# Kernel optimization log

Hardware: AMD Instinct MI355X
Metric: run time of the kernel (lower is better)

## Reference

```python
import jax, jax.numpy as jnp
import numpy as np

K = 9          # neighbors kept after dilation
DILATION = 2   # top-k runs with K*DILATION then strided slice
EPS = 1e-12    # F.normalize eps


def setup_inputs() -> dict:
    key = jax.random.key(0)
    # x: [B, C, N, 1] feature map over N points with C channels
    x = jax.random.normal(key, (2, 64, 8192, 1), dtype=jnp.float32)
    return {"x": x}


def reference(x):
    k_total = K * DILATION
    # L2-normalize along channel dim (F.normalize(x, p=2, dim=1))
    norm = jnp.sqrt(jnp.sum(x * x, axis=1, keepdims=True))
    xn = x / jnp.maximum(norm, EPS)
    # [B, C, N, 1] -> [B, N, C]
    pts = jnp.transpose(jnp.squeeze(xn, -1), (0, 2, 1))
    B, N, _ = pts.shape
    # pairwise squared distances: ||xi||^2 - 2 xi.xj + ||xj||^2  -> [B, N, N]
    sq = jnp.sum(pts * pts, axis=-1, keepdims=True)            # [B, N, 1]
    dist = sq - 2.0 * jnp.einsum('bnc,bmc->bnm', pts, pts) + jnp.swapaxes(sq, 1, 2)
    # k nearest = top-k of negated distance (matches torch.topk(-dist, k))
    _, nn_idx = jax.lax.top_k(-dist, k_total)                  # [B, N, k_total] int32
    center_idx = jnp.broadcast_to(jnp.arange(N, dtype=nn_idx.dtype)[None, :, None],
                                  (B, N, k_total))
    edge_index = jnp.stack([nn_idx, center_idx], axis=0)       # [2, B, N, k_total]
    # dilation (non-stochastic path): strided slice over neighbor dim
    return edge_index[:, :, :, ::DILATION]                     # [2, B, N, K]
```

## Files before the change

kernel.cpp:

```cpp
#include <hip/hip_runtime.h>


#define NPTS  8192
#define CHN   64
#define NB    2
#define KF    18
#define KC    8
#define KM    16
#define KOUT  9
#define NPART 4
#define TPB   32

typedef unsigned u32;
typedef unsigned short u16;
typedef unsigned long long u64;
typedef __attribute__((ext_vector_type(4))) unsigned u32x4;
typedef __attribute__((ext_vector_type(8))) short bf16x8;
typedef __attribute__((ext_vector_type(4))) float f32x4;

__device__ __forceinline__ u32 umin32(u32 a, u32 b) { return a < b ? a : b; }

__device__ __forceinline__ u32 mono32(float f) {
  const u32 u = __float_as_uint(f);
  const u32 s = (u32)((int)u >> 31);
  return u ^ (s | 0x80000000u);
}

__device__ __forceinline__ u32 med3u(u32 a, u32 b, u32 c) {
  u32 r;
  asm("v_med3_u32 %0, %1, %2, %3" : "=v"(r) : "v"(a), "v"(b), "v"(c));
  return r;
}

template <int KK>
__device__ __forceinline__ void insmm(u32 key, u32 (&d)[KK]) {
#pragma unroll
  for (int k = KK - 1; k >= 1; --k) d[k] = med3u(d[k - 1], d[k], key);
  d[0] = umin32(d[0], key);
}

template <int KK>
__device__ __forceinline__ void ins64(u64 key, u64 (&d)[KK]) {
  if (key < d[KK - 1]) {
#pragma unroll
    for (int k = KK - 1; k >= 1; --k) {
      const bool up = d[k - 1] > key;
      const bool here = (!up) && (d[k] > key);
      d[k] = up ? d[k - 1] : (here ? key : d[k]);
    }
    if (d[0] > key) d[0] = key;
  }
}

__device__ __forceinline__ void gload_lds16(const u32* g, u32* l) {
  __builtin_amdgcn_global_load_lds(
      (const __attribute__((address_space(1))) u32*)g,
      (__attribute__((address_space(3))) u32*)l, 16, 0, 0);
}

__device__ __forceinline__ void np_normalize(const float* __restrict__ xb,
                                             float (&v)[CHN]) {
  float ss = 0.f;
#pragma unroll
  for (int c = 0; c < CHN; ++c) {
    v[c] = xb[(size_t)c * NPTS];
    ss = __fadd_rn(ss, __fmul_rn(v[c], v[c]));
  }
  const float den = fmaxf(__fsqrt_rn(ss), 1e-12f);
#pragma unroll
  for (int c = 0; c < CHN; ++c) v[c] = __fdiv_rn(v[c], den);
}

__global__ __launch_bounds__(128) void prep_kernel(
    const float* __restrict__ x, u32* __restrict__ hib, u32* __restrict__ lob,
    u32* __restrict__ w16b, float* __restrict__ sq) {
  const int b = blockIdx.x >> 6;
  const int n = ((blockIdx.x & 63) << 7) + threadIdx.x;
  const int g = (b << 13) + n;
  float v[CHN];
  np_normalize(x + (size_t)b * CHN * NPTS + n, v);
  float r[8];
#pragma unroll
  for (int j = 0; j < 8; ++j) r[j] = __fmul_rn(v[j], v[j]);
#pragma unroll
  for (int blk = 1; blk < 8; ++blk)
#pragma unroll
    for (int j = 0; j < 8; ++j)
      r[j] = __fadd_rn(r[j], __fmul_rn(v[8 * blk + j], v[8 * blk + j]));
  const float t0 = __fadd_rn(r[0], r[1]);
  const float t1 = __fadd_rn(r[2], r[3]);
  const float t2 = __fadd_rn(r[4], r[5]);
  const float t3 = __fadd_rn(r[6], r[7]);
  sq[g] = __fadd_rn(__fadd_rn(t0, t1), __fadd_rn(t2, t3));
  u32* hd = hib + (size_t)g * 32;
  u32* ld = lob + (size_t)g * 32;
  u32* wd = w16b + (size_t)g * 32;
  const int key = n & 7;
#pragma unroll
  for (int q = 0; q < 8; ++q) {
    u32 h[4], l[4], w[4];
#pragma unroll
    for (int p2 = 0; p2 < 4; ++p2) {
      const float a = v[8 * q + 2 * p2];
      const float c = v[8 * q + 2 * p2 + 1];
      const u32 ba = __float_as_uint(a), bc = __float_as_uint(c);
      const float la = a - __uint_as_float(ba & 0xffff0000u);
      const float lc = c - __uint_as_float(bc & 0xffff0000u);
      h[p2] = __builtin_amdgcn_perm(bc, ba, 0x07060302u);
      l[p2] = __builtin_amdgcn_perm(__float_as_uint(lc), __float_as_uint(la),
                                    0x07060302u);
      w[p2] = __builtin_amdgcn_perm(bc, ba, 0x05040100u);
    }
    const int pq = (q ^ key) << 2;
    *(u32x4*)(hd + pq) = (u32x4){h[0], h[1], h[2], h[3]};
    *(u32x4*)(ld + pq) = (u32x4){l[0], l[1], l[2], l[3]};
    *(u32x4*)(wd + pq) = (u32x4){w[0], w[1], w[2], w[3]};
  }
}

__global__ __launch_bounds__(256, 2) void knn_part_kernel(
    const u32* __restrict__ hib, const u32* __restrict__ lob,
    const float* __restrict__ sq, u16* __restrict__ cand) {
  __shared__ __align__(16) u32 pw[4][2][2048];

  const int tid = threadIdx.x;
  const int vb = ((blockIdx.x & 7) << 7) + (blockIdx.x >> 3);
  const int part = vb >> 8;
  const int w = vb & 255;
  const int b = w >> 7;
  const int qbase = (w & 127) << 6;
  const int t_lo = part << 5;
  const u32* __restrict__ hb_ = hib + ((size_t)b << 18);
  const u32* __restrict__ lb_ = lob + ((size_t)b << 18);
  const float* __restrict__ sqb = sq + (b << 13);

  const int lane = tid & 63, wid = tid >> 6;
  const int qoff = (wid & 1) << 5;
  const int moff = (wid >> 1) << 5;
  const int l15 = lane & 15;
  const int h4 = lane >> 4;
  const int sw = l15 & 7;
  const int lofs = lane << 2;

#define STAGE(BUF, TILE)                                                     \
  {                                                                          \
    const u32* sH_ = hb_ + ((size_t)(TILE) << 11) + (moff << 5);             \
    const u32* sL_ = lb_ + ((size_t)(TILE) << 11) + (moff << 5);             \
    u32* bp_ = &pw[wid][(BUF)][0];                                           \
    gload_lds16(sH_ + lofs, bp_ + lofs);                                     \
    gload_lds16(sH_ + 256 + lofs, bp_ + 256 + lofs);                         \
    gload_lds16(sH_ + 512 + lofs, bp_ + 512 + lofs);                         \
    gload_lds16(sH_ + 768 + lofs, bp_ + 768 + lofs);                         \
    gload_lds16(sL_ + lofs, bp_ + 1024 + lofs);                              \
    gload_lds16(sL_ + 256 + lofs, bp_ + 1280 + lofs);                        \
    gload_lds16(sL_ + 512 + lofs, bp_ + 1536 + lofs);                        \
    gload_lds16(sL_ + 768 + lofs, bp_ + 1792 + lofs);                        \
  }

  STAGE(0, t_lo)
  float sqn0 = sqb[(t_lo << 6) + moff + l15];
  float sqn1 = sqb[(t_lo << 6) + moff + 16 + l15];

  bf16x8 ah[2][2], al[2][2];
#pragma unroll
  for (int g = 0; g < 2; ++g)
#pragma unroll
    for (int s = 0; s < 2; ++s) {
      const int row = qbase + qoff + (g << 4) + l15;
      const int off = row * 32 + ((((s << 2) + h4) ^ sw) << 2);
      u32x4 hv = *(const u32x4*)(hb_ + off);
      u32x4 lv = *(const u32x4*)(lb_ + off);
      hv.x ^= 0x80008000u; hv.y ^= 0x80008000u;
      hv.z ^= 0x80008000u; hv.w ^= 0x80008000u;
      lv.x ^= 0x80008000u; lv.y ^= 0x80008000u;
      lv.z ^= 0x80008000u; lv.w ^= 0x80008000u;
      ah[g][s] = __builtin_bit_cast(bf16x8, hv);
      al[g][s] = __builtin_bit_cast(bf16x8, lv);
    }
  asm volatile("s_waitcnt vmcnt(0)" ::: "memory");
  __builtin_amdgcn_sched_barrier(0);

  u32 d[2][4][KC];
#pragma unroll
  for (int g = 0; g < 2; ++g)
#pragma unroll
    for (int i = 0; i < 4; ++i)
#pragma unroll
      for (int k = 0; k < KC; ++k) d[g][i][k] = 0xffffffffu;

  for (int tau = 0; tau < TPB; ++tau) {
    const int cur = tau & 1;
    const float sq0 = sqn0, sq1 = sqn1;
    if (tau + 1 < TPB) {
      STAGE(cur ^ 1, t_lo + tau + 1)
      sqn0 = sqb[((t_lo + tau + 1) << 6) + moff + l15];
      sqn1 = sqb[((t_lo + tau + 1) << 6) + moff + 16 + l15];
      asm volatile("s_waitcnt vmcnt(10)" ::: "memory");
    } else {
      asm volatile("s_waitcnt vmcnt(0)" ::: "memory");
    }
    __builtin_amdgcn_sched_barrier(0);

    const u32* ppc = &pw[wid][cur][0];
#pragma unroll
    for (int f = 0; f < 2; ++f) {
      const float sqm = ((f ? sq1 : sq0) + 2.f) * 0.5f;
      const int rloc = (f << 4) + l15;
      f32x4 acc[2];
      acc[0] = (f32x4){sqm, sqm, sqm, sqm};
      acc[1] = acc[0];
#pragma unroll
      for (int s = 0; s < 2; ++s) {
        const u32* hp = ppc + rloc * 32 + ((((s << 2) + h4) ^ sw) << 2);
        const bf16x8 bh = __builtin_bit_cast(bf16x8, *(const u32x4*)hp);
        const bf16x8 bl = __builtin_bit_cast(bf16x8, *(const u32x4*)(hp + 1024));
        acc[0] = __builtin_amdgcn_mfma_f32_16x16x32_bf16(ah[0][s], bh, acc[0], 0, 0, 0);
        acc[1] = __builtin_amdgcn_mfma_f32_16x16x32_bf16(ah[1][s], bh, acc[1], 0, 0, 0);
        acc[0] = __builtin_amdgcn_mfma_f32_16x16x32_bf16(al[0][s], bh, acc[0], 0, 0, 0);
        acc[1] = __builtin_amdgcn_mfma_f32_16x16x32_bf16(al[1][s], bh, acc[1], 0, 0, 0);
        acc[0] = __builtin_amdgcn_mfma_f32_16x16x32_bf16(ah[0][s], bl, acc[0], 0, 0, 0);
        acc[1] = __builtin_amdgcn_mfma_f32_16x16x32_bf16(ah[1][s], bl, acc[1], 0, 0, 0);
      }
      const u32 lidx = (u32)((tau << 6) + moff + rloc);
#pragma unroll
      for (int g = 0; g < 2; ++g)
#pragma unroll
        for (int i = 0; i < 4; ++i) {
          const u32 keyv = (__float_as_uint(acc[g][i]) & 0xfffff000u) | lidx;
          insmm<KC>(keyv, d[g][i]);
        }
    }
  }
#undef STAGE
  __syncthreads();

  u32* mg = &pw[0][0][0];
  const int stream = ((wid >> 1) << 4) + l15;
  const int rcb = ((wid & 1) << 4) + (h4 << 2);
#pragma unroll
  for (int chunk = 0; chunk < 2; ++chunk) {
#pragma unroll
    for (int i = 0; i < 4; ++i) {
      u32* wr = mg + ((rcb + i) * 32 + stream) * 8;
      u32x4 a, c;
      a.x = d[chunk][i][0]; a.y = d[chunk][i][1];
      a.z = d[chunk][i][2]; a.w = d[chunk][i][3];
      c.x = d[chunk][i][4]; c.y = d[chunk][i][5];
      c.z = d[chunk][i][6]; c.w = d[chunk][i][7];
      *(u32x4*)wr = a;
      *(u32x4*)(wr + 4) = c;
    }
    __syncthreads();
    {
      const int rowc = tid >> 3, oct = tid & 7;
      u32* base = mg + rowc * 256 + oct * 32;
      u32 m1[14];
#pragma unroll
      for (int k = 0; k < 14; ++k) m1[k] = 0xffffffffu;
#pragma unroll
      for (int j = 0; j < 8; ++j) {
        const u32x4 k4 = *(const u32x4*)(base + (j << 2));
        insmm<14>(k4.x, m1);
        insmm<14>(k4.y, m1);
        insmm<14>(k4.z, m1);
        insmm<14>(k4.w, m1);
      }
#pragma unroll
      for (int k = 0; k < 14; ++k) base[k] = m1[k];
    }
    __syncthreads();
    if (tid < 64) {
      const int rowc = tid >> 1, half = tid & 1;
      u32* rb = mg + rowc * 256 + half * 128;
      u32 m2[KM];
#pragma unroll
      for (int k = 0; k < KM; ++k) m2[k] = 0xffffffffu;
#pragma unroll
      for (int o = 0; o < 4; ++o) {
        const u32* p = rb + o * 32;
        for (int j = 0; j < 14; ++j) insmm<KM>(p[j], m2);
      }
#pragma unroll
      for (int k = 0; k < KM; ++k) rb[k] = m2[k];
    }
    __syncthreads();
    if (tid < 32) {
      u32 m3[KM];
#pragma unroll
      for (int k = 0; k < KM; ++k) m3[k] = 0xffffffffu;
      const u32* p0 = mg + tid * 256;
      for (int j = 0; j < KM; ++j) insmm<KM>(p0[j], m3);
      const u32* p1 = mg + tid * 256 + 128;
      for (int j = 0; j < KM; ++j) insmm<KM>(p1[j], m3);
      const int row = ((tid >> 4) << 5) + (chunk << 4) + (tid & 15);
      const int rg = (b << 13) + qbase + row;
      u16* cw = cand + (size_t)rg * (NPART * KM) + part * KM;
#pragma unroll
      for (int k = 0; k < KM; ++k)
        cw[k] = (u16)((part << 11) + (m3[k] & 0xfffu));
    }
    __syncthreads();
  }
}

__global__ __launch_bounds__(512) void finalize_kernel(
    const u32* __restrict__ hib, const u32* __restrict__ w16b,
    const float* __restrict__ sq, const u16* __restrict__ cand,
    int* __restrict__ out) {
  __shared__ u64 ex[64 * 66];
  __shared__ u64 hf[128 * 19];
  const int tid = threadIdx.x;
  const int rl = tid >> 3, sub = tid & 7;
  const int row = (blockIdx.x << 6) + rl;
  const int b = row >> 13;
  const int n = row & 8191;
  const float sqn = sq[row];
  const float* __restrict__ sqb = sq + (b << 13);
  const u32* __restrict__ hb_ = hib + ((size_t)b << 18);
  const u32* __restrict__ wb_ = w16b + ((size_t)b << 18);
  float vq[CHN];
  {
    const u32* hq = hb_ + ((size_t)n << 5);
    const u32* wq = wb_ + ((size_t)n << 5);
    const int key = n & 7;
#pragma unroll
    for (int q = 0; q < 8; ++q) {
      const int pq = (q ^ key) << 2;
      const u32x4 hw = *(const u32x4*)(hq + pq);
      const u32x4 ww = *(const u32x4*)(wq + pq);
      const u32 hv[4] = {hw.x, hw.y, hw.z, hw.w};
      const u32 wv[4] = {ww.x, ww.y, ww.z, ww.w};
#pragma unroll
      for (int p2 = 0; p2 < 4; ++p2) {
        vq[8 * q + 2 * p2] =
            __uint_as_float((hv[p2] << 16) | (wv[p2] & 0xffffu));
        vq[8 * q + 2 * p2 + 1] =
            __uint_as_float((hv[p2] & 0xffff0000u) | (wv[p2] >> 16));
      }
    }
  }
  const u16* __restrict__ cr = cand + (size_t)row * 64 + sub * 8;
  u64* exw = ex + rl * 66 + sub * 8;
  for (int j = 0; j < 8; ++j) {
    const int ix = cr[j];
    const u32* hp = hb_ + ((size_t)ix << 5);
    const u32* wp = wb_ + ((size_t)ix << 5);
    const int key = ix & 7;
    float dot = 0.f;
#pragma unroll
    for (int q = 0; q < 8; ++q) {
      const int pq = (q ^ key) << 2;
      const u32x4 hw = *(const u32x4*)(hp + pq);
      const u32x4 ww = *(const u32x4*)(wp + pq);
      const u32 hv[4] = {hw.x, hw.y, hw.z, hw.w};
      const u32 wv[4] = {ww.x, ww.y, ww.z, ww.w};
#pragma unroll
      for (int p2 = 0; p2 < 4; ++p2) {
        const float a = __uint_as_float((hv[p2] << 16) | (wv[p2] & 0xffffu));
        const float c = __uint_as_float((hv[p2] & 0xffff0000u) | (wv[p2] >> 16));
        dot = __fadd_rn(dot, __fmul_rn(vq[8 * q + 2 * p2], a));
        dot = __fadd_rn(dot, __fmul_rn(vq[8 * q + 2 * p2 + 1], c));
      }
    }
    const float dist =
        __fadd_rn(__fsub_rn(sqn, __fmul_rn(2.0f, dot)), sqb[ix]);
    exw[j] = ((u64)mono32(dist) << 32) | (u32)ix;
  }
  __syncthreads();
  if (tid < 128) {
    const int r2 = tid >> 1, hv = tid & 1;
    u64 m18[KF];
#pragma unroll
    for (int k = 0; k < KF; ++k) m18[k] = ~0ull;
    const u64* p = ex + r2 * 66 + hv * 32;
    for (int j = 0; j < 32; ++j) ins64<KF>(p[j], m18);
    u64* wr = hf + tid * 19;
#pragma unroll
    for (int k = 0; k < KF; ++k) wr[k] = m18[k];
  }
  __syncthreads();
  if (tid < 64) {
    u64 m18[KF];
#pragma unroll
    for (int k = 0; k < KF; ++k) m18[k] = ~0ull;
    const u64* p0 = hf + (tid << 1) * 19;
    const u64* p1 = hf + ((tid << 1) + 1) * 19;
    for (int j = 0; j < KF; ++j) ins64<KF>(p0[j], m18);
    for (int j = 0; j < KF; ++j) ins64<KF>(p1[j], m18);
    const int row2 = (blockIdx.x << 6) + tid;
    int* o0 = out + (size_t)row2 * KOUT;
    int* o1 = o0 + NB * NPTS * KOUT;
#pragma unroll
    for (int k = 0; k < KOUT; ++k) {
      o0[k] = (int)(m18[2 * k] & 0xffffffffu);
      o1[k] = row2 & 8191;
    }
  }
}

extern "C" void kernel_launch(void* const* d_in, const int* in_sizes, int n_in,
                              void* d_out, int out_size, void* d_ws, size_t ws_size,
                              hipStream_t stream) {
  const float* x = (const float*)d_in[0];
  u32* hib = (u32*)d_ws;
  u32* lob = hib + (size_t)NB * NPTS * 32;
  u32* w16b = lob + (size_t)NB * NPTS * 32;
  float* sqg = (float*)(w16b + (size_t)NB * NPTS * 32);
  u16* cand = (u16*)(sqg + NB * NPTS);
  int* out = (int*)d_out;
  prep_kernel<<<dim3(128), dim3(128), 0, stream>>>(x, hib, lob, w16b, sqg);
  knn_part_kernel<<<dim3(1024), dim3(256), 0, stream>>>(hib, lob, sqg, cand);
  finalize_kernel<<<dim3(256), dim3(512), 0, stream>>>(hib, w16b, sqg, cand, out);
}
```

Before: 210.1 us.

## Load candidate tiles directly from global memory into registers, dropping LDS staging

Removes the double-buffered global_load_lds staging of candidate point tiles and the XOR swizzle layout. MFMA B operands and squared norms are now loaded straight from global memory (L2-cached) into registers each iteration. The shared buffer shrinks to the merge area only, and launch bounds allow three blocks per CU to raise occupancy. The cost is that global load latency is no longer hidden by explicit prefetch, and every wave re-reads the tiles through the cache.

```diff
diff --git a/kernel.cpp b/kernel.cpp
--- a/kernel.cpp
+++ b/kernel.cpp
@@ -50,12 +50,6 @@
     }
     if (d[0] > key) d[0] = key;
   }
-}
-
-__device__ __forceinline__ void gload_lds16(const u32* g, u32* l) {
-  __builtin_amdgcn_global_load_lds(
-      (const __attribute__((address_space(1))) u32*)g,
-      (__attribute__((address_space(3))) u32*)l, 16, 0, 0);
 }
 
 __device__ __forceinline__ void np_normalize(const float* __restrict__ xb,
@@ -95,7 +89,6 @@
   u32* hd = hib + (size_t)g * 32;
   u32* ld = lob + (size_t)g * 32;
   u32* wd = w16b + (size_t)g * 32;
-  const int key = n & 7;
 #pragma unroll
   for (int q = 0; q < 8; ++q) {
     u32 h[4], l[4], w[4];
@@ -111,17 +104,17 @@
                                     0x07060302u);
       w[p2] = __builtin_amdgcn_perm(bc, ba, 0x05040100u);
     }
-    const int pq = (q ^ key) << 2;
+    const int pq = q << 2;
     *(u32x4*)(hd + pq) = (u32x4){h[0], h[1], h[2], h[3]};
     *(u32x4*)(ld + pq) = (u32x4){l[0], l[1], l[2], l[3]};
     *(u32x4*)(wd + pq) = (u32x4){w[0], w[1], w[2], w[3]};
   }
 }
 
-__global__ __launch_bounds__(256, 2) void knn_part_kernel(
+__global__ __launch_bounds__(256, 3) void knn_part_kernel(
     const u32* __restrict__ hib, const u32* __restrict__ lob,
     const float* __restrict__ sq, u16* __restrict__ cand) {
-  __shared__ __align__(16) u32 pw[4][2][2048];
+  __shared__ __align__(16) u32 mg[8192];
 
   const int tid = threadIdx.x;
   const int vb = ((blockIdx.x & 7) << 7) + (blockIdx.x >> 3);
@@ -139,27 +132,6 @@
   const int moff = (wid >> 1) << 5;
   const int l15 = lane & 15;
   const int h4 = lane >> 4;
-  const int sw = l15 & 7;
-  const int lofs = lane << 2;
-
-#define STAGE(BUF, TILE)                                                     \
-  {                                                                          \
-    const u32* sH_ = hb_ + ((size_t)(TILE) << 11) + (moff << 5);             \
-    const u32* sL_ = lb_ + ((size_t)(TILE) << 11) + (moff << 5);             \
-    u32* bp_ = &pw[wid][(BUF)][0];                                           \
-    gload_lds16(sH_ + lofs, bp_ + lofs);                                     \
-    gload_lds16(sH_ + 256 + lofs, bp_ + 256 + lofs);                         \
-    gload_lds16(sH_ + 512 + lofs, bp_ + 512 + lofs);                         \
-    gload_lds16(sH_ + 768 + lofs, bp_ + 768 + lofs);                         \
-    gload_lds16(sL_ + lofs, bp_ + 1024 + lofs);                              \
-    gload_lds16(sL_ + 256 + lofs, bp_ + 1280 + lofs);                        \
-    gload_lds16(sL_ + 512 + lofs, bp_ + 1536 + lofs);                        \
-    gload_lds16(sL_ + 768 + lofs, bp_ + 1792 + lofs);                        \
-  }
-
-  STAGE(0, t_lo)
-  float sqn0 = sqb[(t_lo << 6) + moff + l15];
-  float sqn1 = sqb[(t_lo << 6) + moff + 16 + l15];
 
   bf16x8 ah[2][2], al[2][2];
 #pragma unroll
@@ -167,7 +139,7 @@
 #pragma unroll
     for (int s = 0; s < 2; ++s) {
       const int row = qbase + qoff + (g << 4) + l15;
-      const int off = row * 32 + ((((s << 2) + h4) ^ sw) << 2);
+      const int off = row * 32 + (((s << 2) + h4) << 2);
       u32x4 hv = *(const u32x4*)(hb_ + off);
       u32x4 lv = *(const u32x4*)(lb_ + off);
       hv.x ^= 0x80008000u; hv.y ^= 0x80008000u;
@@ -177,8 +149,6 @@
       ah[g][s] = __builtin_bit_cast(bf16x8, hv);
       al[g][s] = __builtin_bit_cast(bf16x8, lv);
     }
-  asm volatile("s_waitcnt vmcnt(0)" ::: "memory");
-  __builtin_amdgcn_sched_barrier(0);
 
   u32 d[2][4][KC];
 #pragma unroll
@@ -189,31 +159,30 @@
       for (int k = 0; k < KC; ++k) d[g][i][k] = 0xffffffffu;
 
   for (int tau = 0; tau < TPB; ++tau) {
-    const int cur = tau & 1;
-    const float sq0 = sqn0, sq1 = sqn1;
-    if (tau + 1 < TPB) {
-      STAGE(cur ^ 1, t_lo + tau + 1)
-      sqn0 = sqb[((t_lo + tau + 1) << 6) + moff + l15];
-      sqn1 = sqb[((t_lo + tau + 1) << 6) + moff + 16 + l15];
-      asm volatile("s_waitcnt vmcnt(10)" ::: "memory");
-    } else {
-      asm volatile("s_waitcnt vmcnt(0)" ::: "memory");
-    }
-    __builtin_amdgcn_sched_barrier(0);
-
-    const u32* ppc = &pw[wid][cur][0];
+    const int tile = t_lo + tau;
+    const float sqm0 = (sqb[(tile << 6) + moff + l15] + 2.f) * 0.5f;
+    const float sqm1 = (sqb[(tile << 6) + moff + 16 + l15] + 2.f) * 0.5f;
+    u32x4 vbh[2][2], vbl[2][2];
 #pragma unroll
     for (int f = 0; f < 2; ++f) {
-      const float sqm = ((f ? sq1 : sq0) + 2.f) * 0.5f;
-      const int rloc = (f << 4) + l15;
+#pragma unroll
+      for (int s = 0; s < 2; ++s) {
+        const int m_l = moff + (f << 4) + l15;
+        const size_t off = ((size_t)tile << 11) + m_l * 32 + (((s << 2) + h4) << 2);
+        vbh[f][s] = *(const u32x4*)(hb_ + off);
+        vbl[f][s] = *(const u32x4*)(lb_ + off);
+      }
+    }
+#pragma unroll
+    for (int f = 0; f < 2; ++f) {
+      const float sqm = f ? sqm1 : sqm0;
       f32x4 acc[2];
       acc[0] = (f32x4){sqm, sqm, sqm, sqm};
       acc[1] = acc[0];
 #pragma unroll
       for (int s = 0; s < 2; ++s) {
-        const u32* hp = ppc + rloc * 32 + ((((s << 2) + h4) ^ sw) << 2);
-        const bf16x8 bh = __builtin_bit_cast(bf16x8, *(const u32x4*)hp);
-        const bf16x8 bl = __builtin_bit_cast(bf16x8, *(const u32x4*)(hp + 1024));
+        const bf16x8 bh = __builtin_bit_cast(bf16x8, vbh[f][s]);
+        const bf16x8 bl = __builtin_bit_cast(bf16x8, vbl[f][s]);
         acc[0] = __builtin_amdgcn_mfma_f32_16x16x32_bf16(ah[0][s], bh, acc[0], 0, 0, 0);
         acc[1] = __builtin_amdgcn_mfma_f32_16x16x32_bf16(ah[1][s], bh, acc[1], 0, 0, 0);
         acc[0] = __builtin_amdgcn_mfma_f32_16x16x32_bf16(al[0][s], bh, acc[0], 0, 0, 0);
@@ -221,7 +190,7 @@
         acc[0] = __builtin_amdgcn_mfma_f32_16x16x32_bf16(ah[0][s], bl, acc[0], 0, 0, 0);
         acc[1] = __builtin_amdgcn_mfma_f32_16x16x32_bf16(ah[1][s], bl, acc[1], 0, 0, 0);
       }
-      const u32 lidx = (u32)((tau << 6) + moff + rloc);
+      const u32 lidx = (u32)((tau << 6) + moff + (f << 4) + l15);
 #pragma unroll
       for (int g = 0; g < 2; ++g)
 #pragma unroll
@@ -231,10 +200,7 @@
         }
     }
   }
-#undef STAGE
-  __syncthreads();
-
-  u32* mg = &pw[0][0][0];
+
   const int stream = ((wid >> 1) << 4) + l15;
   const int rcb = ((wid & 1) << 4) + (h4 << 2);
 #pragma unroll
@@ -322,10 +288,9 @@
   {
     const u32* hq = hb_ + ((size_t)n << 5);
     const u32* wq = wb_ + ((size_t)n << 5);
-    const int key = n & 7;
 #pragma unroll
     for (int q = 0; q < 8; ++q) {
-      const int pq = (q ^ key) << 2;
+      const int pq = q << 2;
       const u32x4 hw = *(const u32x4*)(hq + pq);
       const u32x4 ww = *(const u32x4*)(wq + pq);
       const u32 hv[4] = {hw.x, hw.y, hw.z, hw.w};
@@ -345,11 +310,10 @@
     const int ix = cr[j];
     const u32* hp = hb_ + ((size_t)ix << 5);
     const u32* wp = wb_ + ((size_t)ix << 5);
-    const int key = ix & 7;
     float dot = 0.f;
 #pragma unroll
     for (int q = 0; q < 8; ++q) {
-      const int pq = (q ^ key) << 2;
+      const int pq = q << 2;
       const u32x4 hw = *(const u32x4*)(hp + pq);
       const u32x4 ww = *(const u32x4*)(wp + pq);
       const u32 hv[4] = {hw.x, hw.y, hw.z, hw.w};
```

New measurement: 254.9 us. +21.3%, slower.
